# Kernel optimization log

Measured on AMD Instinct MI355X. Metric: run time of the kernel, lower is better.

## Reference

```python
import jax, jax.numpy as jnp
import numpy as np
from jax import lax

B, S, C = 32, 4096, 512   # batch, seq_len, input_dim
P, K = 3, 10              # pairs_per_fan_in, max_fan_in


def setup_inputs() -> dict:
    key = jax.random.key(0)
    keys = jax.random.split(key, K + 1)
    inp = {"x": jax.random.normal(keys[0], (B, S, C), dtype=jnp.float32)}
    for k in range(1, K + 1):
        # WIO layout: (kernel_width=k, in_channels=C, out_channels=P)
        fan_in = C * k
        scale = 1.0 / np.sqrt(fan_in)  # kaiming-uniform-ish scale
        inp[f"w{k}"] = scale * jax.random.normal(keys[k], (k, C, P), dtype=jnp.float32)
    return inp


def _causal_conv(x, w):
    # x: (B, S, C), w: (k, C, P) -> (B, S, P); left-pad k-1 == torch padding=k-1 then [:, :, :S]
    k = w.shape[0]
    return lax.conv_general_dilated(
        x, w, window_strides=(1,), padding=[(k - 1, 0)],
        dimension_numbers=("NWC", "WIO", "NWC"))


def reference(x, w1, w2, w3, w4, w5, w6, w7, w8, w9, w10) -> jnp.ndarray:
    ws = (w1, w2, w3, w4, w5, w6, w7, w8, w9, w10)
    # ReLU each causal conv output, concat along feature dim -> (B, S, K*P)
    parts = [jax.nn.relu(_causal_conv(x, w)) for w in ws]
    return jnp.concatenate(parts, axis=-1)
```

## Files before the change

### kernel.cpp

```cpp
#include <hip/hip_runtime.h>

typedef _Float16 half8 __attribute__((ext_vector_type(8)));
typedef __attribute__((ext_vector_type(4))) float f32x4;

#define C_DIM 512
#define S_DIM 4096
#define NCOL 165
#define NCOLP 176
#define M_OUT 64
#define ROWS 80
#define BK 32
#define NCHUNK 16
#define RJ 9
#define BUFSZ 12288
#define YST 180
#define YSLOT 2880

struct WP { const float* w[10]; };

__global__ __launch_bounds__(256) void prep_kernel(WP wp, _Float16* bt, float4* zbuf) {
  if (blockIdx.x == NCOLP * C_DIM / 256) {
    zbuf[threadIdx.x] = make_float4(0.f, 0.f, 0.f, 0.f);
    return;
  }
  int idx = blockIdx.x * 256 + threadIdx.x;
  int col = idx >> 9;
  int c = idx & 511;
  float v = 0.f;
  if (col < NCOL) {
    int kw = 1, base = 0;
    while (col >= base + 3 * kw) { base += 3 * kw; ++kw; }
    int rem = col - base;
    int t = rem / 3, p = rem - 3 * t;
    v = wp.w[kw - 1][(t * C_DIM + c) * 3 + p];
  }
  bt[col * C_DIM + c] = (_Float16)v;
}

__device__ __forceinline__ void gld16(const void* g, void* l) {
  __builtin_amdgcn_global_load_lds(
      (const __attribute__((address_space(1))) unsigned int*)(const unsigned int*)g,
      (__attribute__((address_space(3))) unsigned int*)(unsigned int*)l, 16, 0, 0);
}

__device__ __forceinline__ void wait_vm3() {
  __asm__ volatile("s_waitcnt vmcnt(3)" ::: "memory");
}
__device__ __forceinline__ void barrier_lgkm() {
  __asm__ volatile("s_waitcnt lgkmcnt(0)\n\ts_barrier" ::: "memory");
}

__global__ __launch_bounds__(256, 3) void conv_kernel(const float* __restrict__ x,
                                                      const _Float16* __restrict__ bt,
                                                      const float* __restrict__ zbuf,
                                                      float* __restrict__ out) {
  __shared__ __align__(16) unsigned char smem[3 * BUFSZ];
  float* Ys = (float*)smem;

  const int tid = threadIdx.x;
  const int b = blockIdx.x >> 6;
  const int tile = blockIdx.x & 63;
  const int s0 = tile * M_OUT;
  const int sBase = s0 - 16;
  const int wave = tid >> 6;
  const int lane = tid & 63;
  const int l15 = lane & 15;
  const int quad = lane >> 4;
  const int wnu = __builtin_amdgcn_readfirstlane(wave);
  const int n0 = wave * 3;
  const int nmine = (wave < 3) ? 3 : 2;

  const half8* bptr[3];
#pragma unroll
  for (int nn = 0; nn < 3; ++nn) {
    int cr = (n0 + nn) * 16 + l15;
    bptr[nn] = (const half8*)&bt[(nn < nmine ? cr : l15) * C_DIM + quad * 8];
  }

  const char* asrc[3];
#pragma unroll
  for (int i = 0; i < 3; ++i) {
    int t = wave * 3 + i;
    int sigma = t * 64 + lane;
    int row = sigma / RJ;
    int j = sigma - row * RJ;
    int s = sBase + row;
    bool ok = (j < 8) && (row < ROWS) && (s >= 0);
    asrc[i] = ok ? (const char*)&x[((size_t)(b * S_DIM + s)) * C_DIM + j * 4]
                 : (const char*)zbuf + lane * 16;
  }
  const int ldst = wnu * 3;

  f32x4 acc[5][3];
#pragma unroll
  for (int m = 0; m < 5; ++m)
#pragma unroll
    for (int n = 0; n < 3; ++n) acc[m][n] = (f32x4){0.f, 0.f, 0.f, 0.f};

#pragma unroll
  for (int i = 0; i < 3; ++i)
    gld16(asrc[i], smem + (ldst + i) * 1024);
#pragma unroll
  for (int i = 0; i < 3; ++i)
    gld16(asrc[i] + 128, smem + BUFSZ + (ldst + i) * 1024);
  wait_vm3();
  barrier_lgkm();

#pragma unroll
  for (int ch = 0; ch < NCHUNK; ++ch) {
    const int cb = ch % 3;
    const int nb = (ch + 2) % 3;
    half8 bfr[3];
#pragma unroll
    for (int nn = 0; nn < 3; ++nn)
      if (nn < nmine) bfr[nn] = bptr[nn][ch * 4];
    if (ch < NCHUNK - 2) {
#pragma unroll
      for (int i = 0; i < 3; ++i)
        gld16(asrc[i] + (ch + 2) * 128, smem + nb * BUFSZ + (ldst + i) * 1024);
    }
    const float* Af = (const float*)(smem + cb * BUFSZ);
#pragma unroll
    for (int m = 0; m < 5; ++m) {
      const float* rp = Af + (m * 16 + l15) * (RJ * 4) + quad * 8;
      f32x4 a0 = *(const f32x4*)rp;
      f32x4 a1 = *(const f32x4*)(rp + 4);
      half8 ah = {(_Float16)a0[0], (_Float16)a0[1], (_Float16)a0[2], (_Float16)a0[3],
                  (_Float16)a1[0], (_Float16)a1[1], (_Float16)a1[2], (_Float16)a1[3]};
#pragma unroll
      for (int nn = 0; nn < 3; ++nn)
        if (nn < nmine)
          acc[m][nn] = __builtin_amdgcn_mfma_f32_16x16x32_f16(ah, bfr[nn], acc[m][nn], 0, 0, 0);
    }
    wait_vm3();
    barrier_lgkm();
  }

  __syncthreads();

#pragma unroll
  for (int i = 1; i <= 4; ++i) {
    if (i == 1) {
#pragma unroll
      for (int nn = 0; nn < 3; ++nn)
        if (nn < nmine)
#pragma unroll
          for (int r = 0; r < 4; ++r)
            Ys[0 * YSLOT + (quad * 4 + r) * YST + (n0 + nn) * 16 + l15] = acc[0][nn][r];
    }
#pragma unroll
    for (int nn = 0; nn < 3; ++nn)
      if (nn < nmine)
#pragma unroll
        for (int r = 0; r < 4; ++r)
          Ys[(i & 1) * YSLOT + (quad * 4 + r) * YST + (n0 + nn) * 16 + l15] = acc[i][nn][r];
    __syncthreads();
    for (int o = tid; o < 480; o += 256) {
      int r = o / 30;
      int j = o - 30 * r;
      int kw = j / 3 + 1;
      int p = j - (kw - 1) * 3;
      int base = 3 * (kw * (kw - 1)) / 2;
      float sum = 0.f;
      for (int d = 0; d < kw; ++d) {
        int rr = r - d;
        int slot = (rr >= 0) ? (i & 1) : ((i ^ 1) & 1);
        int lr = (rr >= 0) ? rr : (16 + rr);
        int colv = base + (kw - 1 - d) * 3 + p;
        sum += Ys[slot * YSLOT + lr * YST + colv];
      }
      int s = s0 + 16 * (i - 1) + r;
      out[((size_t)(b * S_DIM + s)) * 30 + j] = fmaxf(sum, 0.f);
    }
    __syncthreads();
  }
}

extern "C" void kernel_launch(void* const* d_in, const int* in_sizes, int n_in,
                              void* d_out, int out_size, void* d_ws, size_t ws_size,
                              hipStream_t stream) {
  const float* x = (const float*)d_in[0];
  WP wp;
  for (int k = 0; k < 10; ++k) wp.w[k] = (const float*)d_in[k + 1];
  _Float16* bt = (_Float16*)d_ws;
  float4* zbuf = (float4*)((char*)d_ws + NCOLP * C_DIM * 2);
  prep_kernel<<<NCOLP * C_DIM / 256 + 1, 256, 0, stream>>>(wp, bt, zbuf);
  conv_kernel<<<32 * (S_DIM / M_OUT), 256, 0, stream>>>(x, bt, (const float*)zbuf,
                                                        (float*)d_out);
}
```

Before: 407.1 us.

## Deepen A-tile prefetch to four LDS buffers and prefetch B fragments two chunks ahead

```diff
diff --git a/kernel.cpp b/kernel.cpp
--- a/kernel.cpp
+++ b/kernel.cpp
@@ -13,6 +13,7 @@
 #define NCHUNK 16
 #define RJ 9
 #define BUFSZ 12288
+#define NBUF 4
 #define YST 180
 #define YSLOT 2880
 
@@ -43,8 +44,9 @@
       (__attribute__((address_space(3))) unsigned int*)(unsigned int*)l, 16, 0, 0);
 }
 
-__device__ __forceinline__ void wait_vm3() {
-  __asm__ volatile("s_waitcnt vmcnt(3)" ::: "memory");
+template <int N>
+__device__ __forceinline__ void wait_vm() {
+  __asm__ volatile("s_waitcnt vmcnt(%0)" ::"i"(N) : "memory");
 }
 __device__ __forceinline__ void barrier_lgkm() {
   __asm__ volatile("s_waitcnt lgkmcnt(0)\n\ts_barrier" ::: "memory");
@@ -54,7 +56,7 @@
                                                       const _Float16* __restrict__ bt,
                                                       const float* __restrict__ zbuf,
                                                       float* __restrict__ out) {
-  __shared__ __align__(16) unsigned char smem[3 * BUFSZ];
+  __shared__ __align__(16) unsigned char smem[NBUF * BUFSZ];
   float* Ys = (float*)smem;
 
   const int tid = threadIdx.x;
@@ -97,29 +99,34 @@
 #pragma unroll
     for (int n = 0; n < 3; ++n) acc[m][n] = (f32x4){0.f, 0.f, 0.f, 0.f};
 
-#pragma unroll
-  for (int i = 0; i < 3; ++i)
-    gld16(asrc[i], smem + (ldst + i) * 1024);
-#pragma unroll
-  for (int i = 0; i < 3; ++i)
-    gld16(asrc[i] + 128, smem + BUFSZ + (ldst + i) * 1024);
-  wait_vm3();
+  half8 breg[3][3];
+#pragma unroll
+  for (int nn = 0; nn < 3; ++nn)
+    if (nn < nmine) breg[0][nn] = bptr[nn][0];
+#pragma unroll
+  for (int nn = 0; nn < 3; ++nn)
+    if (nn < nmine) breg[1][nn] = bptr[nn][4];
+#pragma unroll
+  for (int c = 0; c < 3; ++c)
+#pragma unroll
+    for (int i = 0; i < 3; ++i)
+      gld16(asrc[i] + c * 128, smem + c * BUFSZ + (ldst + i) * 1024);
+  wait_vm<6>();
   barrier_lgkm();
 
 #pragma unroll
   for (int ch = 0; ch < NCHUNK; ++ch) {
-    const int cb = ch % 3;
-    const int nb = (ch + 2) % 3;
-    half8 bfr[3];
-#pragma unroll
-    for (int nn = 0; nn < 3; ++nn)
-      if (nn < nmine) bfr[nn] = bptr[nn][ch * 4];
-    if (ch < NCHUNK - 2) {
+    if (ch + 2 < NCHUNK) {
+#pragma unroll
+      for (int nn = 0; nn < 3; ++nn)
+        if (nn < nmine) breg[(ch + 2) % 3][nn] = bptr[nn][(ch + 2) * 4];
+    }
+    if (ch + 3 < NCHUNK) {
 #pragma unroll
       for (int i = 0; i < 3; ++i)
-        gld16(asrc[i] + (ch + 2) * 128, smem + nb * BUFSZ + (ldst + i) * 1024);
-    }
-    const float* Af = (const float*)(smem + cb * BUFSZ);
+        gld16(asrc[i] + (ch + 3) * 128, smem + ((ch + 3) % NBUF) * BUFSZ + (ldst + i) * 1024);
+    }
+    const float* Af = (const float*)(smem + (ch % NBUF) * BUFSZ);
 #pragma unroll
     for (int m = 0; m < 5; ++m) {
       const float* rp = Af + (m * 16 + l15) * (RJ * 4) + quad * 8;
@@ -130,10 +137,14 @@
 #pragma unroll
       for (int nn = 0; nn < 3; ++nn)
         if (nn < nmine)
-          acc[m][nn] = __builtin_amdgcn_mfma_f32_16x16x32_f16(ah, bfr[nn], acc[m][nn], 0, 0, 0);
-    }
-    wait_vm3();
-    barrier_lgkm();
+          acc[m][nn] =
+              __builtin_amdgcn_mfma_f32_16x16x32_f16(ah, breg[ch % 3][nn], acc[m][nn], 0, 0, 0);
+    }
+    if (ch == 0) wait_vm<9>();
+    else if (ch <= 12) wait_vm<12>();
+    else if (ch == 13) wait_vm<9>();
+    else if (ch == 14) wait_vm<3>();
+    if (ch < NCHUNK - 1) barrier_lgkm();
   }
 
   __syncthreads();
```

Result: no change. 400.9 us (-1.5%).

## Load activations directly from global into registers, dropping LDS triple-buffer staging

Applied to the files above, without the earlier changes.

```diff
diff --git a/kernel.cpp b/kernel.cpp
--- a/kernel.cpp
+++ b/kernel.cpp
@@ -8,21 +8,13 @@
 #define NCOL 165
 #define NCOLP 176
 #define M_OUT 64
-#define ROWS 80
-#define BK 32
 #define NCHUNK 16
-#define RJ 9
-#define BUFSZ 12288
 #define YST 180
 #define YSLOT 2880
 
 struct WP { const float* w[10]; };
 
-__global__ __launch_bounds__(256) void prep_kernel(WP wp, _Float16* bt, float4* zbuf) {
-  if (blockIdx.x == NCOLP * C_DIM / 256) {
-    zbuf[threadIdx.x] = make_float4(0.f, 0.f, 0.f, 0.f);
-    return;
-  }
+__global__ __launch_bounds__(256) void prep_kernel(WP wp, _Float16* bt) {
   int idx = blockIdx.x * 256 + threadIdx.x;
   int col = idx >> 9;
   int c = idx & 511;
@@ -37,25 +29,10 @@
   bt[col * C_DIM + c] = (_Float16)v;
 }
 
-__device__ __forceinline__ void gld16(const void* g, void* l) {
-  __builtin_amdgcn_global_load_lds(
-      (const __attribute__((address_space(1))) unsigned int*)(const unsigned int*)g,
-      (__attribute__((address_space(3))) unsigned int*)(unsigned int*)l, 16, 0, 0);
-}
-
-__device__ __forceinline__ void wait_vm3() {
-  __asm__ volatile("s_waitcnt vmcnt(3)" ::: "memory");
-}
-__device__ __forceinline__ void barrier_lgkm() {
-  __asm__ volatile("s_waitcnt lgkmcnt(0)\n\ts_barrier" ::: "memory");
-}
-
-__global__ __launch_bounds__(256, 3) void conv_kernel(const float* __restrict__ x,
+__global__ __launch_bounds__(256, 4) void conv_kernel(const float* __restrict__ x,
                                                       const _Float16* __restrict__ bt,
-                                                      const float* __restrict__ zbuf,
                                                       float* __restrict__ out) {
-  __shared__ __align__(16) unsigned char smem[3 * BUFSZ];
-  float* Ys = (float*)smem;
+  __shared__ __align__(16) float Ys[2 * YSLOT];
 
   const int tid = threadIdx.x;
   const int b = blockIdx.x >> 6;
@@ -66,9 +43,9 @@
   const int lane = tid & 63;
   const int l15 = lane & 15;
   const int quad = lane >> 4;
-  const int wnu = __builtin_amdgcn_readfirstlane(wave);
   const int n0 = wave * 3;
   const int nmine = (wave < 3) ? 3 : 2;
+  const bool t0 = (tile == 0);
 
   const half8* bptr[3];
 #pragma unroll
@@ -77,19 +54,13 @@
     bptr[nn] = (const half8*)&bt[(nn < nmine ? cr : l15) * C_DIM + quad * 8];
   }
 
-  const char* asrc[3];
+  const float* aP[5];
 #pragma unroll
-  for (int i = 0; i < 3; ++i) {
-    int t = wave * 3 + i;
-    int sigma = t * 64 + lane;
-    int row = sigma / RJ;
-    int j = sigma - row * RJ;
-    int s = sBase + row;
-    bool ok = (j < 8) && (row < ROWS) && (s >= 0);
-    asrc[i] = ok ? (const char*)&x[((size_t)(b * S_DIM + s)) * C_DIM + j * 4]
-                 : (const char*)zbuf + lane * 16;
+  for (int m = 0; m < 5; ++m) {
+    int s = sBase + m * 16 + l15;
+    if (s < 0) s = 0;
+    aP[m] = &x[((size_t)(b * S_DIM + s)) * C_DIM + quad * 8];
   }
-  const int ldst = wnu * 3;
 
   f32x4 acc[5][3];
 #pragma unroll
@@ -97,34 +68,18 @@
 #pragma unroll
     for (int n = 0; n < 3; ++n) acc[m][n] = (f32x4){0.f, 0.f, 0.f, 0.f};
 
-#pragma unroll
-  for (int i = 0; i < 3; ++i)
-    gld16(asrc[i], smem + (ldst + i) * 1024);
-#pragma unroll
-  for (int i = 0; i < 3; ++i)
-    gld16(asrc[i] + 128, smem + BUFSZ + (ldst + i) * 1024);
-  wait_vm3();
-  barrier_lgkm();
-
-#pragma unroll
+#pragma unroll 4
   for (int ch = 0; ch < NCHUNK; ++ch) {
-    const int cb = ch % 3;
-    const int nb = (ch + 2) % 3;
     half8 bfr[3];
 #pragma unroll
     for (int nn = 0; nn < 3; ++nn)
       if (nn < nmine) bfr[nn] = bptr[nn][ch * 4];
-    if (ch < NCHUNK - 2) {
-#pragma unroll
-      for (int i = 0; i < 3; ++i)
-        gld16(asrc[i] + (ch + 2) * 128, smem + nb * BUFSZ + (ldst + i) * 1024);
-    }
-    const float* Af = (const float*)(smem + cb * BUFSZ);
 #pragma unroll
     for (int m = 0; m < 5; ++m) {
-      const float* rp = Af + (m * 16 + l15) * (RJ * 4) + quad * 8;
-      f32x4 a0 = *(const f32x4*)rp;
-      f32x4 a1 = *(const f32x4*)(rp + 4);
+      if (m == 0 && t0) continue;
+      const f32x4* ap = (const f32x4*)(aP[m] + ch * 32);
+      f32x4 a0 = ap[0];
+      f32x4 a1 = ap[1];
       half8 ah = {(_Float16)a0[0], (_Float16)a0[1], (_Float16)a0[2], (_Float16)a0[3],
                   (_Float16)a1[0], (_Float16)a1[1], (_Float16)a1[2], (_Float16)a1[3]};
 #pragma unroll
@@ -132,11 +87,7 @@
         if (nn < nmine)
           acc[m][nn] = __builtin_amdgcn_mfma_f32_16x16x32_f16(ah, bfr[nn], acc[m][nn], 0, 0, 0);
     }
-    wait_vm3();
-    barrier_lgkm();
   }
-
-  __syncthreads();
 
 #pragma unroll
   for (int i = 1; i <= 4; ++i) {
@@ -183,8 +134,6 @@
   WP wp;
   for (int k = 0; k < 10; ++k) wp.w[k] = (const float*)d_in[k + 1];
   _Float16* bt = (_Float16*)d_ws;
-  float4* zbuf = (float4*)((char*)d_ws + NCOLP * C_DIM * 2);
-  prep_kernel<<<NCOLP * C_DIM / 256 + 1, 256, 0, stream>>>(wp, bt, zbuf);
-  conv_kernel<<<32 * (S_DIM / M_OUT), 256, 0, stream>>>(x, bt, (const float*)zbuf,
-                                                        (float*)d_out);
+  prep_kernel<<<NCOLP * C_DIM / 256, 256, 0, stream>>>(wp, bt);
+  conv_kernel<<<32 * (S_DIM / M_OUT), 256, 0, stream>>>(x, bt, (float*)d_out);
 }
```

Result: slower. 489.2 us (+20.2%).
